# Kernel tuning notes

Measured on AMD Instinct MI355X. Metric: run time of the kernel, lower is better.

Reference implementation:

```python
import jax, jax.numpy as jnp
import numpy as np

B, S, A, E, H, V, P = 128, 256, 8, 300, 300, 50000, 3


def _gru(x, wih, whh, bih, bhh):
    """torch.nn.GRU (single layer, batch_first) with gate order r,z,n."""
    h0 = jnp.zeros((x.shape[0], whh.shape[1]), x.dtype)

    def step(h, xt):
        gi = xt @ wih.T + bih            # [B,3H]
        gh = h @ whh.T + bhh
        ir, iz, in_ = jnp.split(gi, 3, axis=-1)
        hr, hz, hn = jnp.split(gh, 3, axis=-1)
        r = jax.nn.sigmoid(ir + hr)
        z = jax.nn.sigmoid(iz + hz)
        n = jnp.tanh(in_ + r * hn)
        hnew = (1.0 - z) * n + z * h
        return hnew, hnew

    _, ys = jax.lax.scan(step, h0, jnp.swapaxes(x, 0, 1))  # scan over time
    return jnp.swapaxes(ys, 0, 1)                          # [B,S,H]


def setup_inputs() -> dict:
    key = jax.random.key(0)
    ks = jax.random.split(key, 16)
    rn = lambda k, shape, s=0.05: jax.random.normal(k, shape, jnp.float32) * s
    z = lambda *shape: jnp.zeros(shape, jnp.float32)
    return {
        "embed_table": rn(ks[0], (V, E), 1.0),
        "w1": rn(ks[1], (E, 3 * E)), "b1": z(E),
        "w2": rn(ks[2], (1, E)),
        "wm": rn(ks[3], (E, E)), "bm": z(E),
        "wd": rn(ks[4], (P, E)), "bd": z(P),
        "wih_l": rn(ks[5], (3 * H, E)), "whh_l": rn(ks[6], (3 * H, H)),
        "bih_l": z(3 * H), "bhh_l": z(3 * H),
        "wih_r": rn(ks[7], (3 * H, E)), "whh_r": rn(ks[8], (3 * H, H)),
        "bih_r": z(3 * H), "bhh_r": z(3 * H),
        "wml": rn(ks[9], (1, H)), "bml": z(1),
        "wmr": rn(ks[10], (1, H)), "bmr": z(1),
        # all token ids >= 1 so lengths are exactly the padded length (packing == identity)
        "text_raw_indices": jax.random.randint(ks[11], (B, S), 1, V),
        "aspect_indices": jax.random.randint(ks[12], (B, A), 1, V),
        "x_l": jax.random.randint(ks[13], (B, S), 1, V),
        "x_r": jax.random.randint(ks[14], (B, S), 1, V),
    }


def _forward(embed_table, w1, b1, w2, wm, bm, wd, bd,
             wih_l, whh_l, bih_l, bhh_l, wih_r, whh_r, bih_r, bhh_r,
             wml, bml, wmr, bmr, text, aspect, xl, xr):
    memory_len = jnp.sum(text != 0, -1)    # [B]
    aspect_len = jnp.sum(aspect != 0, -1)
    left_len = jnp.sum(xl != 0, -1)

    v_a = jnp.sum(embed_table[aspect], 1) / aspect_len[:, None].astype(jnp.float32)  # [B,E]
    memory = embed_table[text]             # [B,S,E]

    # ---- context attention (attention #1), fully vectorized ----
    ctx_l = _gru(embed_table[xl], wih_l, whh_l, bih_l, bhh_l)  # [B,S,H]
    ctx_r = _gru(embed_table[xr], wih_r, whh_r, bih_r, bhh_r)
    attn_l = jax.nn.sigmoid(jnp.einsum('bsh,h->bs', ctx_l, wml[0]) + bml[0]) + 0.5  # [B,S]
    attn_r = jax.nn.sigmoid(jnp.einsum('bsh,h->bs', ctx_r, wmr[0]) + bmr[0]) + 0.5

    idx = jnp.arange(S)[None, :]                      # [1,S]
    a_start = (left_len - aspect_len)[:, None]        # [B,1]
    a_end = left_len[:, None]
    # attn_r reversed over the first aspect_end positions: attn_rr[i,t] = attn_r[i, a_end-1-t]
    attn_rr = jnp.take_along_axis(attn_r, jnp.clip(a_end - 1 - idx, 0, S - 1), axis=1)
    # attn_l shifted by aspect_start: attn_ls[i,t] = attn_l[i, t - a_start]
    attn_ls = jnp.take_along_axis(attn_l, jnp.clip(idx - a_start, 0, S - 1), axis=1)
    w = jnp.where(idx < a_start, attn_rr,
                  jnp.where(idx < a_end, (attn_rr + attn_ls) * 0.5, attn_ls))
    w = jnp.where(idx < memory_len[:, None], w, 1.0)  # untouched past memory_len
    memory = memory * w[..., None]

    v_s = jnp.sum(memory, 1) / memory_len[:, None].astype(jnp.float32)  # [B,E]

    # ---- content attention (attention #2) ----
    feat = jnp.concatenate([memory,
                            jnp.broadcast_to(v_a[:, None, :], memory.shape),
                            jnp.broadcast_to(v_s[:, None, :], memory.shape)], -1)  # [B,S,3E]
    c = jnp.tanh(feat @ w1.T + b1) @ w2.T             # [B,S,1]
    alpha = jax.nn.softmax(c[..., 0], axis=1)         # [B,S]
    v_ts = jnp.einsum('bse,bs->be', memory, alpha)    # [B,E]

    v_ns = v_ts + v_s                                 # dropout is identity at eval
    v_ms = jnp.tanh(v_ns @ wm.T + bm)
    return jax.nn.softmax(v_ms @ wd.T + bd, axis=-1)  # [B,P]


def reference(embed_table, w1, b1, w2, wm, bm, wd, bd,
              wih_l, whh_l, bih_l, bhh_l, wih_r, whh_r, bih_r, bhh_r,
              wml, bml, wmr, bmr, text_raw_indices, aspect_indices, x_l, x_r):
    return _forward(embed_table, w1, b1, w2, wm, bm, wd, bd,
                    wih_l, whh_l, bih_l, bhh_l, wih_r, whh_r, bih_r, bhh_r,
                    wml, bml, wmr, bmr, text_raw_indices, aspect_indices, x_l, x_r)
```

## Files before the change

### kernel.cpp

```cpp
#include <hip/hip_runtime.h>
#include <hip/hip_bf16.h>
#include <math.h>

#define Bd 128
#define Sd 256
#define Ad 8
#define Ed 300
#define Hd 300
#define EP 320
#define Pd 3
#define UC 5
#define BG 8

typedef __attribute__((ext_vector_type(8))) short bfrag;
typedef __attribute__((ext_vector_type(4))) float f32x4;
typedef __attribute__((ext_vector_type(4))) int i32x4;

#define OFF_LENS   0u
#define OFF_FLAGS  4096u
#define OFF_VA     8192u
#define OFF_VS     172032u
#define OFF_U      335872u
#define OFF_ATTN   499712u
#define OFF_ALPHA  761856u
#define OFF_C      892928u
#define OFF_HF     1024000u
#define OFF_PART   1351680u
#define OFF_WF     11837440u
#define OFF_W1B    14295040u
#define OFF_XF     14499840u
#define OFF_MEMW   14499840u
#define WS_NEEDED  56442880u

__device__ __forceinline__ unsigned short f2bf(float f) {
    __hip_bfloat16 h = __float2bfloat16(f);
    return *reinterpret_cast<unsigned short*>(&h);
}
__device__ __forceinline__ float bf2f(unsigned short u) {
    __hip_bfloat16 h = *reinterpret_cast<__hip_bfloat16*>(&u);
    return __bfloat162float(h);
}
__device__ __forceinline__ float sigm(float x) {
    return __builtin_amdgcn_rcpf(1.f + __expf(-x));
}
__device__ __forceinline__ float fast_tanh(float x) {
    x = fminf(fmaxf(x, -15.f), 15.f);
    float e = __expf(2.f * x);
    return (e - 1.f) * __builtin_amdgcn_rcpf(e + 1.f);
}

__device__ __forceinline__ bfrag l2_load16b(const void* p) {
    bfrag v;
    asm volatile("global_load_dwordx4 %0, %1, off sc0"
                 : "=v"(v) : "v"(p) : "memory");
    return v;
}
__device__ __forceinline__ void l2_store16(void* p, i32x4 v) {
    asm volatile("global_store_dwordx4 %0, %1, off sc0"
                 :: "v"(p), "v"(v) : "memory");
}

__global__ void k_lengths(const int* __restrict__ text, const int* __restrict__ aspect,
                          const int* __restrict__ xl, int* __restrict__ lens) {
    int b = blockIdx.x;
    __shared__ int red[3];
    if (threadIdx.x < 3) red[threadIdx.x] = 0;
    __syncthreads();
    int t = threadIdx.x;
    if (t < Sd) {
        if (text[b*Sd + t] != 0) atomicAdd(&red[0], 1);
        if (xl[b*Sd + t]  != 0) atomicAdd(&red[2], 1);
    }
    if (t < Ad) { if (aspect[b*Ad + t] != 0) atomicAdd(&red[1], 1); }
    __syncthreads();
    if (t < 3) lens[b*4 + t] = red[t];
}

__global__ void k_va(const float* __restrict__ embed, const int* __restrict__ aspect,
                     const int* __restrict__ lens, float* __restrict__ va) {
    int b = blockIdx.x;
    __shared__ int aidx[Ad];
    if (threadIdx.x < Ad) aidx[threadIdx.x] = aspect[b*Ad + threadIdx.x];
    __syncthreads();
    float inv = 1.0f / (float)lens[b*4+1];
    for (int e = threadIdx.x; e < EP; e += blockDim.x) {
        float s = 0.f;
        if (e < Ed) {
            for (int a = 0; a < Ad; ++a) s += embed[(size_t)aidx[a]*Ed + e];
        }
        va[b*EP + e] = s * inv;
    }
}

__global__ void k_xf(const float* __restrict__ embed, const int* __restrict__ xl,
                     const int* __restrict__ xr, unsigned short* __restrict__ XF) {
    int side = blockIdx.x >> 8;
    int t = blockIdx.x & 255;
    const int* xs = side ? xr : xl;
    __shared__ int rows_s[Bd];
    if (threadIdx.x < Bd) rows_s[threadIdx.x] = xs[threadIdx.x*Sd + t];
    __syncthreads();
    unsigned short* dst = XF + ((size_t)(side*Sd + t))*40960;
    for (int v8 = threadIdx.x; v8 < 5120; v8 += 256) {
        int idx = v8 << 3;
        int bt = idx / 5120;
        int r1 = idx - bt*5120;
        int kt = r1 >> 9;
        int r2 = r1 & 511;
        int lane = r2 >> 3;
        int b = bt*16 + (lane & 15);
        int kk = kt*32 + (lane >> 4)*8;
        const float* src = embed + (size_t)rows_s[b]*Ed + kk;
        unsigned short tmp[8];
        if (kk + 8 <= Ed) {
            f32x4 f0 = *(const f32x4*)(src);
            f32x4 f1 = *(const f32x4*)(src + 4);
            #pragma unroll
            for (int j = 0; j < 4; ++j) { tmp[j] = f2bf(f0[j]); tmp[4+j] = f2bf(f1[j]); }
        } else {
            #pragma unroll
            for (int j = 0; j < 8; ++j)
                tmp[j] = (kk + j < Ed) ? f2bf(src[j]) : (unsigned short)0;
        }
        *(bfrag*)(dst + idx) = *(const bfrag*)tmp;
    }
}

__global__ void k_wfrag(const float* __restrict__ wih_l, const float* __restrict__ whh_l,
                        const float* __restrict__ wih_r, const float* __restrict__ whh_r,
                        unsigned short* __restrict__ WF) {
    int bid = blockIdx.x;
    int side = bid / 120;
    int r = bid - side*120;
    int mat = r / 60; r -= mat*60;
    int g = r / 20;
    int ut = r - g*20;
    const float* W = mat ? (side ? whh_r : whh_l) : (side ? wih_r : wih_l);
    unsigned short* dst = WF + (size_t)bid*5120;
    for (int v8 = threadIdx.x; v8 < 640; v8 += 256) {
        int idx = v8 << 3;
        int kt = idx >> 9;
        int r2 = idx & 511;
        int lane = r2 >> 3;
        int unit = ut*16 + (lane & 15);
        int kk = kt*32 + (lane >> 4)*8;
        unsigned short tmp[8];
        if (unit < Hd && kk + 8 <= Ed) {
            const float* src = W + (size_t)(g*Hd + unit)*Ed + kk;
            f32x4 f0 = *(const f32x4*)(src);
            f32x4 f1 = *(const f32x4*)(src + 4);
            #pragma unroll
            for (int j = 0; j < 4; ++j) { tmp[j] = f2bf(f0[j]); tmp[4+j] = f2bf(f1[j]); }
        } else {
            #pragma unroll
            for (int j = 0; j < 8; ++j) {
                float v = (unit < Hd && kk + j < Ed) ? W[(size_t)(g*Hd + unit)*Ed + kk + j] : 0.f;
                tmp[j] = f2bf(v);
            }
        }
        *(bfrag*)(dst + idx) = *(const bfrag*)tmp;
    }
}

__global__ void k_w1conv(const float* __restrict__ w1, unsigned short* __restrict__ w1b) {
    int idx = blockIdx.x*256 + threadIdx.x;
    if (idx >= EP*EP) return;
    int e = idx / EP, k = idx - e*EP;
    float v = (e < Ed && k < Ed) ? w1[(size_t)e*900 + k] : 0.f;
    w1b[idx] = f2bf(v);
}

__global__ __launch_bounds__(256, 1) void k_gru(
        const unsigned short* __restrict__ WF,
        const unsigned short* __restrict__ XF,
        const float* __restrict__ bih_l, const float* __restrict__ bhh_l,
        const float* __restrict__ bih_r, const float* __restrict__ bhh_r,
        const float* __restrict__ wml, const float* __restrict__ wmr,
        unsigned short* __restrict__ HF,
        float* __restrict__ part, int* __restrict__ flags) {
    int bg = blockIdx.x & 7;
    int r8 = blockIdx.x >> 3;
    int side = r8 & 1;
    int uc = r8 >> 1;
    int tid = threadIdx.x;
    int w = tid >> 6, lane = tid & 63, ul = lane & 15, lq = lane >> 4;
    int utg = uc*4 + w;
    int u = utg*16 + ul;

    const float* bih = side ? bih_r : bih_l;
    const float* bhh = side ? bhh_r : bhh_l;
    const float* wmv = side ? wmr : wml;

    float bR=0.f, bZ=0.f, bNI=0.f, bNH=0.f, wml_r=0.f;
    if (u < Hd) {
        bR = bih[u] + bhh[u];
        bZ = bih[Hd+u] + bhh[Hd+u];
        bNI = bih[2*Hd+u];
        bNH = bhh[2*Hd+u];
        wml_r = wmv[u];
    }

    bfrag wI[3][10], wH[3][10];
    #pragma unroll
    for (int g = 0; g < 3; ++g) {
        const unsigned short* pI = WF + ((size_t)((side*2+0)*3+g)*20 + utg)*5120 + lane*8;
        const unsigned short* pH = WF + ((size_t)((side*2+1)*3+g)*20 + utg)*5120 + lane*8;
        #pragma unroll
        for (int kt = 0; kt < 10; ++kt) {
            wI[g][kt] = *(const bfrag*)(pI + kt*512);
            wH[g][kt] = *(const bfrag*)(pH + kt*512);
        }
    }

    __shared__ __align__(16) unsigned short hn_s[1024];
    int* flgL2 = flags + (side*8 + bg)*16;
    int* flgIC = flags + 512 + (side*8 + bg)*16;
    unsigned short* hfb = HF + (size_t)((side*8 + bg)*2)*5120;
    const unsigned short* xbase = XF + ((size_t)side*Sd*8 + bg)*5120 + lane*8;

    bfrag xA[10], xB[10];
    #pragma unroll
    for (int kt = 0; kt < 10; ++kt)
        xA[kt] = *(const bfrag*)(xbase + 0 + kt*512);

    float hreg[4] = {0.f,0.f,0.f,0.f};
    const f32x4 zero4 = {0.f,0.f,0.f,0.f};

#define GRU_STEP(T, XIN, XOUT) do {                                            \
    f32x4 aR = zero4, aZ = zero4, aNI = zero4, aNH = zero4;                    \
    _Pragma("unroll")                                                          \
    for (int kt = 0; kt < 10; ++kt) {                                          \
        aR  = __builtin_amdgcn_mfma_f32_16x16x32_bf16(XIN[kt], wI[0][kt], aR, 0,0,0); \
        aZ  = __builtin_amdgcn_mfma_f32_16x16x32_bf16(XIN[kt], wI[1][kt], aZ, 0,0,0); \
        aNI = __builtin_amdgcn_mfma_f32_16x16x32_bf16(XIN[kt], wI[2][kt], aNI, 0,0,0); \
    }                                                                          \
    if ((T) > 0) {                                                             \
        if (w == 0) {                                                          \
            int iters = 0;                                                     \
            while (true) {                                                     \
                int v = (T);                                                   \
                if (lane < 2*UC)                                               \
                    v = __hip_atomic_fetch_add(flgL2 + lane, 0, __ATOMIC_RELAXED, __HIP_MEMORY_SCOPE_WORKGROUP); \
                if (__all(v >= (T))) break;                                    \
                if (((++iters) & 63) == 0) {                                   \
                    int vv = (T);                                              \
                    if (lane < 2*UC)                                           \
                        vv = __hip_atomic_load(flgIC + lane, __ATOMIC_RELAXED, __HIP_MEMORY_SCOPE_AGENT); \
                    if (__all(vv >= (T))) break;                               \
                }                                                              \
            }                                                                  \
        }                                                                      \
        __syncthreads();                                                       \
    }                                                                          \
    asm volatile("" ::: "memory");                                             \
    const unsigned short* hg = hfb + (size_t)((T) & 1)*5120 + lane*8;          \
    bfrag hf[10];                                                              \
    _Pragma("unroll")                                                          \
    for (int kt = 0; kt < 10; ++kt)                                            \
        hf[kt] = l2_load16b(hg + kt*512);                                      \
    asm volatile("s_waitcnt vmcnt(0)" ::: "memory");                           \
    __builtin_amdgcn_sched_barrier(0);                                         \
    _Pragma("unroll")                                                          \
    for (int kt = 0; kt < 10; ++kt) {                                          \
        aR  = __builtin_amdgcn_mfma_f32_16x16x32_bf16(hf[kt], wH[0][kt], aR, 0,0,0); \
        aZ  = __builtin_amdgcn_mfma_f32_16x16x32_bf16(hf[kt], wH[1][kt], aZ, 0,0,0); \
        aNH = __builtin_amdgcn_mfma_f32_16x16x32_bf16(hf[kt], wH[2][kt], aNH, 0,0,0); \
    }                                                                          \
    {                                                                          \
        int u_local = w*16 + ul;                                               \
        int kt_l = u_local >> 5, ko = u_local & 31;                            \
        _Pragma("unroll")                                                      \
        for (int i = 0; i < 4; ++i) {                                          \
            float rr = sigm(aR[i] + bR);                                       \
            float zz = sigm(aZ[i] + bZ);                                       \
            float nn = fast_tanh(aNI[i] + bNI + rr*(aNH[i] + bNH));            \
            float hv = (1.f - zz)*nn + zz*hreg[i];                             \
            hreg[i] = hv;                                                      \
            int rrow = lq*4 + i;                                               \
            hn_s[kt_l*512 + (rrow + ((ko>>3)<<4))*8 + (ko&7)] = f2bf(hv);      \
        }                                                                      \
    }                                                                          \
    __syncthreads();           \
    if (w < 2) {                                                               \
        unsigned short* hd = hfb + (size_t)(((T)+1) & 1)*5120 + uc*1024;       \
        l2_store16(hd + (size_t)tid*8, ((const i32x4*)hn_s)[tid]);             \
        asm volatile("s_waitcnt vmcnt(0)" ::: "memory");                       \
        if (lane == 0 && (T) < Sd-1) {                                         \
            __hip_atomic_fetch_add(flgL2 + uc*2 + w, 1, __ATOMIC_RELAXED, __HIP_MEMORY_SCOPE_WORKGROUP); \
            __hip_atomic_store(flgIC + uc*2 + w, (T)+1, __ATOMIC_RELAXED, __HIP_MEMORY_SCOPE_AGENT); \
        }                                                                      \
    }                                                                          \
    {                                                                          \
        int tn = ((T)+1 < Sd) ? (T)+1 : Sd-1;                                  \
        const unsigned short* xp = xbase + (size_t)tn*40960;                   \
        _Pragma("unroll")                                                      \
        for (int kt = 0; kt < 10; ++kt)                                        \
            XOUT[kt] = *(const bfrag*)(xp + kt*512);                           \
    }                                                                          \
    _Pragma("unroll")                                                          \
    for (int i = 0; i < 4; ++i) {                                              \
        float pv = hreg[i] * wml_r;                                            \
        pv += __shfl_xor(pv, 1, 64);                                           \
        pv += __shfl_xor(pv, 2, 64);                                           \
        pv += __shfl_xor(pv, 4, 64);                                           \
        pv += __shfl_xor(pv, 8, 64);                                           \
        if (ul == 0)                                                           \
            part[((size_t)((((side*8+bg)*UC + uc)*4 + w)*16) + lq*4 + i)*Sd + (T)] = pv; \
    }                                                                          \
} while (0)

    #pragma unroll 1
    for (int tt = 0; tt < Sd; tt += 2) {
        GRU_STEP(tt,   xA, xB);
        GRU_STEP(tt+1, xB, xA);
    }
#undef GRU_STEP
}

__global__ void k_attn(const float* __restrict__ part, const float* __restrict__ bml,
                       const float* __restrict__ bmr, float* __restrict__ attn) {
    int side = blockIdx.x >> 7;
    int b = blockIdx.x & 127;
    int bg = b >> 4, r = b & 15;
    int t = threadIdx.x;
    float s = 0.f;
    for (int c = 0; c < UC*4; ++c)
        s += part[((size_t)(((side*8+bg)*UC*4 + c)*16) + r)*Sd + t];
    float bias = side ? bmr[0] : bml[0];
    attn[(size_t)(side*Bd + b)*Sd + t] = sigm(s + bias) + 0.5f;
}

__global__ void k_wmem(const float* __restrict__ embed, const int* __restrict__ text,
                       const float* __restrict__ attn, const int* __restrict__ lens,
                       unsigned short* __restrict__ memw, float* __restrict__ vs) {
    int b = blockIdx.x;
    __shared__ float w_sh[Sd];
    __shared__ int text_s[Sd];
    int memlen = lens[b*4+0], asplen = lens[b*4+1], leftlen = lens[b*4+2];
    int a_start = leftlen - asplen, a_end = leftlen;
    const float* attl = attn + (size_t)b*Sd;
    const float* attr = attn + (size_t)(Bd + b)*Sd;
    if (threadIdx.x < Sd) {
        int i = threadIdx.x;
        int irr = a_end - 1 - i; irr = irr < 0 ? 0 : (irr > Sd-1 ? Sd-1 : irr);
        int ils = i - a_start;   ils = ils < 0 ? 0 : (ils > Sd-1 ? Sd-1 : ils);
        float arr_ = attr[irr], als = attl[ils];
        float w = (i < a_start) ? arr_ : ((i < a_end) ? 0.5f*(arr_+als) : als);
        if (i >= memlen) w = 1.0f;
        w_sh[i] = w;
        text_s[i] = text[b*Sd + i];
    }
    __syncthreads();
    int e = threadIdx.x;
    float acc = 0.f;
    float invm = 1.0f/(float)lens[b*4+0];
    for (int s = 0; s < Sd; ++s) {
        float v = (e < Ed) ? embed[(size_t)text_s[s]*Ed + e] : 0.f;
        float mw = v * w_sh[s];
        memw[((size_t)b*Sd + s)*EP + e] = f2bf(mw);
        acc += mw;
    }
    vs[b*EP + e] = acc * invm;
}

__global__ void k_u(const float* __restrict__ w1, const float* __restrict__ b1,
                    const float* __restrict__ va, const float* __restrict__ vs,
                    float* __restrict__ u) {
    int b = blockIdx.x;
    __shared__ float va_s[Ed], vs_s[Ed];
    for (int k = threadIdx.x; k < Ed; k += blockDim.x) {
        va_s[k] = va[b*EP+k];
        vs_s[k] = vs[b*EP+k];
    }
    __syncthreads();
    int e = threadIdx.x;
    if (e >= EP) return;
    float acc = 0.f;
    if (e < Ed) {
        acc = b1[e];
        const float* r = w1 + (size_t)e*900;
        for (int k = 0; k < Ed; ++k) acc += va_s[k]*r[300+k];
        for (int k = 0; k < Ed; ++k) acc += vs_s[k]*r[600+k];
    }
    u[b*EP + e] = acc;
}

__global__ __launch_bounds__(256) void k_c(const unsigned short* __restrict__ memw,
                   const unsigned short* __restrict__ w1b,
                   const float* __restrict__ u, const float* __restrict__ w2,
                   float* __restrict__ cout) {
    int b = blockIdx.x >> 2;
    int s0 = (blockIdx.x & 3) * 64;
    __shared__ __align__(16) unsigned short A_s[64*328];
    __shared__ __align__(16) unsigned short Bp_s[EP*32];
    __shared__ float u_s[EP], w2_s[EP];
    for (int i = threadIdx.x; i < EP; i += 256) {
        u_s[i] = u[b*EP + i];
        w2_s[i] = (i < Ed) ? w2[i] : 0.f;
    }
    const unsigned short* Ag = memw + ((size_t)b*Sd + s0)*EP;
    for (int c8 = threadIdx.x; c8 < 64*40; c8 += 256) {
        int r = c8 / 40, kk = (c8 - r*40)*8;
        *(bfrag*)(A_s + r*328 + kk) = *(const bfrag*)(Ag + (size_t)r*EP + kk);
    }

    int wave = threadIdx.x >> 6, lane = threadIdx.x & 63;
    int ul = lane & 15, lq = lane >> 4;
    const f32x4 zero4 = {0.f,0.f,0.f,0.f};
    f32x4 acc[20];
    #pragma unroll
    for (int n = 0; n < 20; ++n) acc[n] = zero4;

    for (int kp = 0; kp < 10; ++kp) {
        __syncthreads();
        for (int c8 = threadIdx.x; c8 < EP*4; c8 += 256) {
            int e = c8 >> 2, kk = (c8 & 3)*8;
            *(bfrag*)(Bp_s + e*32 + kk) = *(const bfrag*)(w1b + (size_t)e*EP + kp*32 + kk);
        }
        __syncthreads();
        bfrag a = *(const bfrag*)(A_s + (wave*16 + ul)*328 + kp*32 + lq*8);
        #pragma unroll
        for (int n = 0; n < 20; ++n) {
            bfrag bb = *(const bfrag*)(Bp_s + (n*16 + ul)*32 + lq*8);
            acc[n] = __builtin_amdgcn_mfma_f32_16x16x32_bf16(a, bb, acc[n], 0, 0, 0);
        }
    }
    float cs[4] = {0.f,0.f,0.f,0.f};
    #pragma unroll
    for (int n = 0; n < 20; ++n) {
        int e = n*16 + ul;
        #pragma unroll
        for (int i = 0; i < 4; ++i)
            cs[i] += w2_s[e] * fast_tanh(acc[n][i] + u_s[e]);
    }
    #pragma unroll
    for (int i = 0; i < 4; ++i) {
        float v = cs[i];
        v += __shfl_xor(v, 1, 64); v += __shfl_xor(v, 2, 64);
        v += __shfl_xor(v, 4, 64); v += __shfl_xor(v, 8, 64);
        if (ul == 0) cout[(size_t)b*Sd + s0 + wave*16 + lq*4 + i] = v;
    }
}

__global__ void k_alpha(const float* __restrict__ cin, float* __restrict__ alpha) {
    int b = blockIdx.x;
    int t = threadIdx.x;
    __shared__ float buf[Sd];
    float v = cin[(size_t)b*Sd + t];
    buf[t] = v; __syncthreads();
    for (int s2 = 128; s2 > 0; s2 >>= 1) {
        if (t < s2) buf[t] = fmaxf(buf[t], buf[t+s2]);
        __syncthreads();
    }
    float mx = buf[0];
    __syncthreads();
    float ex = __expf(v - mx);
    buf[t] = ex; __syncthreads();
    for (int s2 = 128; s2 > 0; s2 >>= 1) {
        if (t < s2) buf[t] += buf[t+s2];
        __syncthreads();
    }
    alpha[(size_t)b*Sd + t] = ex / buf[0];
}

__global__ void k_final(const unsigned short* __restrict__ memw, const float* __restrict__ alpha,
                        const float* __restrict__ vs, const float* __restrict__ wm,
                        const float* __restrict__ bm, const float* __restrict__ wd,
                        const float* __restrict__ bd, float* __restrict__ out) {
    int b = blockIdx.x;
    __shared__ float al_s[Sd];
    __shared__ float vns_s[Ed];
    __shared__ float vms_s[Ed];
    __shared__ float lg_s[Pd];
    if (threadIdx.x < Sd) al_s[threadIdx.x] = alpha[(size_t)b*Sd + threadIdx.x];
    __syncthreads();
    int e = threadIdx.x;
    if (e < Ed) {
        float acc = 0.f;
        const unsigned short* mp = memw + (size_t)b*Sd*EP + e;
        for (int s = 0; s < Sd; ++s) acc += bf2f(mp[(size_t)s*EP]) * al_s[s];
        vns_s[e] = acc + vs[b*EP + e];
    }
    __syncthreads();
    if (e < Ed) {
        float acc = bm[e];
        const float* r = wm + (size_t)e*Ed;
        for (int k = 0; k < Ed; ++k) acc += vns_s[k]*r[k];
        vms_s[e] = fast_tanh(acc);
    }
    __syncthreads();
    if (e < Pd) {
        float acc = bd[e];
        const float* r = wd + (size_t)e*Ed;
        for (int k = 0; k < Ed; ++k) acc += vms_s[k]*r[k];
        lg_s[e] = acc;
    }
    __syncthreads();
    if (e < Pd) {
        float m = fmaxf(lg_s[0], fmaxf(lg_s[1], lg_s[2]));
        float den = __expf(lg_s[0]-m)+__expf(lg_s[1]-m)+__expf(lg_s[2]-m);
        out[b*Pd + e] = __expf(lg_s[e]-m)/den;
    }
}

extern "C" void kernel_launch(void* const* d_in, const int* in_sizes, int n_in,
                              void* d_out, int out_size, void* d_ws, size_t ws_size,
                              hipStream_t stream) {
    const float* embed = (const float*)d_in[0];
    const float* w1    = (const float*)d_in[1];
    const float* b1    = (const float*)d_in[2];
    const float* w2    = (const float*)d_in[3];
    const float* wm    = (const float*)d_in[4];
    const float* bm    = (const float*)d_in[5];
    const float* wd    = (const float*)d_in[6];
    const float* bd    = (const float*)d_in[7];
    const float* wih_l = (const float*)d_in[8];
    const float* whh_l = (const float*)d_in[9];
    const float* bih_l = (const float*)d_in[10];
    const float* bhh_l = (const float*)d_in[11];
    const float* wih_r = (const float*)d_in[12];
    const float* whh_r = (const float*)d_in[13];
    const float* bih_r = (const float*)d_in[14];
    const float* bhh_r = (const float*)d_in[15];
    const float* wml   = (const float*)d_in[16];
    const float* bml   = (const float*)d_in[17];
    const float* wmr   = (const float*)d_in[18];
    const float* bmr   = (const float*)d_in[19];
    const int* text    = (const int*)d_in[20];
    const int* aspect  = (const int*)d_in[21];
    const int* xl      = (const int*)d_in[22];
    const int* xr      = (const int*)d_in[23];

    if (ws_size < (size_t)WS_NEEDED) return;
    char* ws = (char*)d_ws;
    int* lens            = (int*)(ws + OFF_LENS);
    int* flags           = (int*)(ws + OFF_FLAGS);
    float* va            = (float*)(ws + OFF_VA);
    float* vs            = (float*)(ws + OFF_VS);
    float* u             = (float*)(ws + OFF_U);
    float* attn          = (float*)(ws + OFF_ATTN);
    float* alpha         = (float*)(ws + OFF_ALPHA);
    float* c             = (float*)(ws + OFF_C);
    unsigned short* HF   = (unsigned short*)(ws + OFF_HF);
    float* part          = (float*)(ws + OFF_PART);
    unsigned short* WF   = (unsigned short*)(ws + OFF_WF);
    unsigned short* w1b  = (unsigned short*)(ws + OFF_W1B);
    unsigned short* XF   = (unsigned short*)(ws + OFF_XF);
    unsigned short* memw = (unsigned short*)(ws + OFF_MEMW);

    hipMemsetAsync(ws + OFF_FLAGS, 0, 4096, stream);
    hipMemsetAsync(ws + OFF_HF, 0, 327680, stream);

    k_lengths<<<128, 256, 0, stream>>>(text, aspect, xl, lens);
    k_va     <<<128, 320, 0, stream>>>(embed, aspect, lens, va);
    k_xf     <<<512, 256, 0, stream>>>(embed, xl, xr, XF);
    k_wfrag  <<<240, 256, 0, stream>>>(wih_l, whh_l, wih_r, whh_r, WF);
    k_w1conv <<<400, 256, 0, stream>>>(w1, w1b);
    k_gru    <<<80, 256, 0, stream>>>(WF, XF, bih_l, bhh_l, bih_r, bhh_r,
                                      wml, wmr, HF, part, flags);
    k_attn   <<<256, 256, 0, stream>>>(part, bml, bmr, attn);
    k_wmem   <<<128, 320, 0, stream>>>(embed, text, attn, lens, memw, vs);
    k_u      <<<128, 320, 0, stream>>>(w1, b1, va, vs, u);
    k_c      <<<512, 256, 0, stream>>>(memw, w1b, u, w2, c);
    k_alpha  <<<128, 256, 0, stream>>>(c, alpha);
    k_final  <<<128, 320, 0, stream>>>(memw, alpha, vs, wm, bm, wd, bd, (float*)d_out);
}
```

Measured before the change: 821.1 us.

## Use single step counter, double-buffered LDS for own hidden slice, direct B loads in k_c

Result: slower. 898.6 us (+9.4%).

```diff
diff --git a/kernel.cpp b/kernel.cpp
--- a/kernel.cpp
+++ b/kernel.cpp
@@ -212,8 +212,12 @@
         }
     }
 
-    __shared__ __align__(16) unsigned short hn_s[1024];
-    int* flgL2 = flags + (side*8 + bg)*16;
+    __shared__ __align__(16) unsigned short hn_s[2][1024];
+    for (int i = tid; i < 512; i += 256)
+        ((unsigned long long*)hn_s)[i] = 0ull;
+    __syncthreads();
+
+    int* ctrL2 = flags + (side*8 + bg)*16 + 10;
     int* flgIC = flags + 512 + (side*8 + bg)*16;
     unsigned short* hfb = HF + (size_t)((side*8 + bg)*2)*5120;
     const unsigned short* xbase = XF + ((size_t)side*Sd*8 + bg)*5120 + lane*8;
@@ -226,7 +230,7 @@
     float hreg[4] = {0.f,0.f,0.f,0.f};
     const f32x4 zero4 = {0.f,0.f,0.f,0.f};
 
-#define GRU_STEP(T, XIN, XOUT) do {                                            \
+#define GRU_STEP(T, PAR, XIN, XOUT) do {                                       \
     f32x4 aR = zero4, aZ = zero4, aNI = zero4, aNH = zero4;                    \
     _Pragma("unroll")                                                          \
     for (int kt = 0; kt < 10; ++kt) {                                          \
@@ -236,15 +240,16 @@
     }                                                                          \
     if ((T) > 0) {                                                             \
         if (w == 0) {                                                          \
+            int target = 10*(T);                                               \
             int iters = 0;                                                     \
             while (true) {                                                     \
-                int v = (T);                                                   \
-                if (lane < 2*UC)                                               \
-                    v = __hip_atomic_fetch_add(flgL2 + lane, 0, __ATOMIC_RELAXED, __HIP_MEMORY_SCOPE_WORKGROUP); \
-                if (__all(v >= (T))) break;                                    \
+                int v = target;                                                \
+                if (lane == 0)                                                 \
+                    v = __hip_atomic_fetch_add(ctrL2, 0, __ATOMIC_RELAXED, __HIP_MEMORY_SCOPE_WORKGROUP); \
+                if (__all(v >= target)) break;                                 \
                 if (((++iters) & 63) == 0) {                                   \
                     int vv = (T);                                              \
-                    if (lane < 2*UC)                                           \
+                    if (lane < 10)                                             \
                         vv = __hip_atomic_load(flgIC + lane, __ATOMIC_RELAXED, __HIP_MEMORY_SCOPE_AGENT); \
                     if (__all(vv >= (T))) break;                               \
                 }                                                              \
@@ -253,11 +258,16 @@
         __syncthreads();                                                       \
     }                                                                          \
     asm volatile("" ::: "memory");                                             \
-    const unsigned short* hg = hfb + (size_t)((T) & 1)*5120 + lane*8;          \
+    const unsigned short* hg = hfb + (size_t)(PAR)*5120 + lane*8;              \
     bfrag hf[10];                                                              \
     _Pragma("unroll")                                                          \
     for (int kt = 0; kt < 10; ++kt)                                            \
-        hf[kt] = l2_load16b(hg + kt*512);                                      \
+        if ((kt >> 1) != uc)                                                   \
+            hf[kt] = l2_load16b(hg + kt*512);                                  \
+    _Pragma("unroll")                                                          \
+    for (int kt = 0; kt < 10; ++kt)                                            \
+        if ((kt >> 1) == uc)                                                   \
+            hf[kt] = *(const bfrag*)(&hn_s[(PAR)^1][(kt & 1)*512 + lane*8]);   \
     asm volatile("s_waitcnt vmcnt(0)" ::: "memory");                           \
     __builtin_amdgcn_sched_barrier(0);                                         \
     _Pragma("unroll")                                                          \
@@ -277,16 +287,16 @@
             float hv = (1.f - zz)*nn + zz*hreg[i];                             \
             hreg[i] = hv;                                                      \
             int rrow = lq*4 + i;                                               \
-            hn_s[kt_l*512 + (rrow + ((ko>>3)<<4))*8 + (ko&7)] = f2bf(hv);      \
+            hn_s[PAR][kt_l*512 + (rrow + ((ko>>3)<<4))*8 + (ko&7)] = f2bf(hv); \
         }                                                                      \
     }                                                                          \
-    __syncthreads();           \
+    __syncthreads();      \
     if (w < 2) {                                                               \
-        unsigned short* hd = hfb + (size_t)(((T)+1) & 1)*5120 + uc*1024;       \
-        l2_store16(hd + (size_t)tid*8, ((const i32x4*)hn_s)[tid]);             \
+        unsigned short* hd = hfb + (size_t)((PAR)^1)*5120 + uc*1024;           \
+        l2_store16(hd + (size_t)tid*8, ((const i32x4*)hn_s[PAR])[tid]);        \
         asm volatile("s_waitcnt vmcnt(0)" ::: "memory");                       \
         if (lane == 0 && (T) < Sd-1) {                                         \
-            __hip_atomic_fetch_add(flgL2 + uc*2 + w, 1, __ATOMIC_RELAXED, __HIP_MEMORY_SCOPE_WORKGROUP); \
+            __hip_atomic_fetch_add(ctrL2, 1, __ATOMIC_RELAXED, __HIP_MEMORY_SCOPE_WORKGROUP); \
             __hip_atomic_store(flgIC + uc*2 + w, (T)+1, __ATOMIC_RELAXED, __HIP_MEMORY_SCOPE_AGENT); \
         }                                                                      \
     }                                                                          \
@@ -311,8 +321,8 @@
 
     #pragma unroll 1
     for (int tt = 0; tt < Sd; tt += 2) {
-        GRU_STEP(tt,   xA, xB);
-        GRU_STEP(tt+1, xB, xA);
+        GRU_STEP(tt,   0, xA, xB);
+        GRU_STEP(tt+1, 1, xB, xA);
     }
 #undef GRU_STEP
 }
@@ -392,7 +402,6 @@
     int b = blockIdx.x >> 2;
     int s0 = (blockIdx.x & 3) * 64;
     __shared__ __align__(16) unsigned short A_s[64*328];
-    __shared__ __align__(16) unsigned short Bp_s[EP*32];
     __shared__ float u_s[EP], w2_s[EP];
     for (int i = threadIdx.x; i < EP; i += 256) {
         u_s[i] = u[b*EP + i];
@@ -403,6 +412,7 @@
         int r = c8 / 40, kk = (c8 - r*40)*8;
         *(bfrag*)(A_s + r*328 + kk) = *(const bfrag*)(Ag + (size_t)r*EP + kk);
     }
+    __syncthreads();
 
     int wave = threadIdx.x >> 6, lane = threadIdx.x & 63;
     int ul = lane & 15, lq = lane >> 4;
@@ -412,18 +422,14 @@
     for (int n = 0; n < 20; ++n) acc[n] = zero4;
 
     for (int kp = 0; kp < 10; ++kp) {
-        __syncthreads();
-        for (int c8 = threadIdx.x; c8 < EP*4; c8 += 256) {
-            int e = c8 >> 2, kk = (c8 & 3)*8;
-            *(bfrag*)(Bp_s + e*32 + kk) = *(const bfrag*)(w1b + (size_t)e*EP + kp*32 + kk);
-        }
-        __syncthreads();
         bfrag a = *(const bfrag*)(A_s + (wave*16 + ul)*328 + kp*32 + lq*8);
+        bfrag bb[20];
         #pragma unroll
-        for (int n = 0; n < 20; ++n) {
-            bfrag bb = *(const bfrag*)(Bp_s + (n*16 + ul)*32 + lq*8);
-            acc[n] = __builtin_amdgcn_mfma_f32_16x16x32_bf16(a, bb, acc[n], 0, 0, 0);
-        }
+        for (int n = 0; n < 20; ++n)
+            bb[n] = *(const bfrag*)(w1b + (size_t)(n*16 + ul)*EP + kp*32 + lq*8);
+        #pragma unroll
+        for (int n = 0; n < 20; ++n)
+            acc[n] = __builtin_amdgcn_mfma_f32_16x16x32_bf16(a, bb[n], acc[n], 0, 0, 0);
     }
     float cs[4] = {0.f,0.f,0.f,0.f};
     #pragma unroll
```

## Fuse small pre/post GRU kernels to cut launches and intermediate buffers

Applied to the files above, without the earlier changes.

Measured after the change: 808.9 us. No clear change (-1.5%).

```diff
diff --git a/kernel.cpp b/kernel.cpp
--- a/kernel.cpp
+++ b/kernel.cpp
@@ -21,8 +21,6 @@
 #define OFF_VA     8192u
 #define OFF_VS     172032u
 #define OFF_U      335872u
-#define OFF_ATTN   499712u
-#define OFF_ALPHA  761856u
 #define OFF_C      892928u
 #define OFF_HF     1024000u
 #define OFF_PART   1351680u
@@ -60,10 +58,12 @@
                  :: "v"(p), "v"(v) : "memory");
 }
 
-__global__ void k_lengths(const int* __restrict__ text, const int* __restrict__ aspect,
-                          const int* __restrict__ xl, int* __restrict__ lens) {
+__global__ void k_lenva(const float* __restrict__ embed, const int* __restrict__ text,
+                        const int* __restrict__ aspect, const int* __restrict__ xl,
+                        int* __restrict__ lens, float* __restrict__ va) {
     int b = blockIdx.x;
     __shared__ int red[3];
+    __shared__ int aidx[Ad];
     if (threadIdx.x < 3) red[threadIdx.x] = 0;
     __syncthreads();
     int t = threadIdx.x;
@@ -71,25 +71,19 @@
         if (text[b*Sd + t] != 0) atomicAdd(&red[0], 1);
         if (xl[b*Sd + t]  != 0) atomicAdd(&red[2], 1);
     }
-    if (t < Ad) { if (aspect[b*Ad + t] != 0) atomicAdd(&red[1], 1); }
+    if (t < Ad) {
+        aidx[t] = aspect[b*Ad + t];
+        if (aidx[t] != 0) atomicAdd(&red[1], 1);
+    }
     __syncthreads();
     if (t < 3) lens[b*4 + t] = red[t];
-}
-
-__global__ void k_va(const float* __restrict__ embed, const int* __restrict__ aspect,
-                     const int* __restrict__ lens, float* __restrict__ va) {
-    int b = blockIdx.x;
-    __shared__ int aidx[Ad];
-    if (threadIdx.x < Ad) aidx[threadIdx.x] = aspect[b*Ad + threadIdx.x];
-    __syncthreads();
-    float inv = 1.0f / (float)lens[b*4+1];
-    for (int e = threadIdx.x; e < EP; e += blockDim.x) {
-        float s = 0.f;
-        if (e < Ed) {
-            for (int a = 0; a < Ad; ++a) s += embed[(size_t)aidx[a]*Ed + e];
-        }
-        va[b*EP + e] = s * inv;
-    }
+    float inv = 1.0f / (float)red[1];
+    int e = t;
+    float s = 0.f;
+    if (e < Ed) {
+        for (int a = 0; a < Ad; ++a) s += embed[(size_t)aidx[a]*Ed + e];
+    }
+    va[b*EP + e] = s * inv;
 }
 
 __global__ void k_xf(const float* __restrict__ embed, const int* __restrict__ xl,
@@ -317,72 +311,69 @@
 #undef GRU_STEP
 }
 
-__global__ void k_attn(const float* __restrict__ part, const float* __restrict__ bml,
-                       const float* __restrict__ bmr, float* __restrict__ attn) {
-    int side = blockIdx.x >> 7;
-    int b = blockIdx.x & 127;
+__global__ void k_awu(const float* __restrict__ part, const float* __restrict__ bml,
+                      const float* __restrict__ bmr, const float* __restrict__ embed,
+                      const int* __restrict__ text, const int* __restrict__ lens,
+                      const float* __restrict__ w1, const float* __restrict__ b1,
+                      const float* __restrict__ va,
+                      unsigned short* __restrict__ memw, float* __restrict__ vs,
+                      float* __restrict__ u) {
+    int b = blockIdx.x;
     int bg = b >> 4, r = b & 15;
-    int t = threadIdx.x;
-    float s = 0.f;
-    for (int c = 0; c < UC*4; ++c)
-        s += part[((size_t)(((side*8+bg)*UC*4 + c)*16) + r)*Sd + t];
-    float bias = side ? bmr[0] : bml[0];
-    attn[(size_t)(side*Bd + b)*Sd + t] = sigm(s + bias) + 0.5f;
-}
-
-__global__ void k_wmem(const float* __restrict__ embed, const int* __restrict__ text,
-                       const float* __restrict__ attn, const int* __restrict__ lens,
-                       unsigned short* __restrict__ memw, float* __restrict__ vs) {
-    int b = blockIdx.x;
+    __shared__ float attl_s[Sd], attr_s[Sd];
     __shared__ float w_sh[Sd];
     __shared__ int text_s[Sd];
+    __shared__ float va_s[EP], vs_s[EP];
+    int t = threadIdx.x;
+
+    if (t < Sd) {
+        float sl = 0.f, sr = 0.f;
+        for (int c = 0; c < UC*4; ++c) {
+            sl += part[((size_t)(((0*8+bg)*UC*4 + c)*16) + r)*Sd + t];
+            sr += part[((size_t)(((1*8+bg)*UC*4 + c)*16) + r)*Sd + t];
+        }
+        attl_s[t] = sigm(sl + bml[0]) + 0.5f;
+        attr_s[t] = sigm(sr + bmr[0]) + 0.5f;
+        text_s[t] = text[b*Sd + t];
+    }
+    va_s[t] = va[b*EP + t];
+    __syncthreads();
+
     int memlen = lens[b*4+0], asplen = lens[b*4+1], leftlen = lens[b*4+2];
     int a_start = leftlen - asplen, a_end = leftlen;
-    const float* attl = attn + (size_t)b*Sd;
-    const float* attr = attn + (size_t)(Bd + b)*Sd;
-    if (threadIdx.x < Sd) {
-        int i = threadIdx.x;
+    if (t < Sd) {
+        int i = t;
         int irr = a_end - 1 - i; irr = irr < 0 ? 0 : (irr > Sd-1 ? Sd-1 : irr);
         int ils = i - a_start;   ils = ils < 0 ? 0 : (ils > Sd-1 ? Sd-1 : ils);
-        float arr_ = attr[irr], als = attl[ils];
+        float arr_ = attr_s[irr], als = attl_s[ils];
         float w = (i < a_start) ? arr_ : ((i < a_end) ? 0.5f*(arr_+als) : als);
         if (i >= memlen) w = 1.0f;
         w_sh[i] = w;
-        text_s[i] = text[b*Sd + i];
-    }
-    __syncthreads();
-    int e = threadIdx.x;
+    }
+    __syncthreads();
+
+    int e = t;
     float acc = 0.f;
-    float invm = 1.0f/(float)lens[b*4+0];
+    float invm = 1.0f/(float)memlen;
     for (int s = 0; s < Sd; ++s) {
         float v = (e < Ed) ? embed[(size_t)text_s[s]*Ed + e] : 0.f;
         float mw = v * w_sh[s];
         memw[((size_t)b*Sd + s)*EP + e] = f2bf(mw);
         acc += mw;
     }
-    vs[b*EP + e] = acc * invm;
-}
-
-__global__ void k_u(const float* __restrict__ w1, const float* __restrict__ b1,
-                    const float* __restrict__ va, const float* __restrict__ vs,
-                    float* __restrict__ u) {
-    int b = blockIdx.x;
-    __shared__ float va_s[Ed], vs_s[Ed];
-    for (int k = threadIdx.x; k < Ed; k += blockDim.x) {
-        va_s[k] = va[b*EP+k];
-        vs_s[k] = vs[b*EP+k];
-    }
-    __syncthreads();
-    int e = threadIdx.x;
-    if (e >= EP) return;
-    float acc = 0.f;
+    float vsv = acc * invm;
+    vs[b*EP + e] = vsv;
+    vs_s[e] = vsv;
+    __syncthreads();
+
+    float accu = 0.f;
     if (e < Ed) {
-        acc = b1[e];
-        const float* r = w1 + (size_t)e*900;
-        for (int k = 0; k < Ed; ++k) acc += va_s[k]*r[300+k];
-        for (int k = 0; k < Ed; ++k) acc += vs_s[k]*r[600+k];
-    }
-    u[b*EP + e] = acc;
+        accu = b1[e];
+        const float* rw = w1 + (size_t)e*900;
+        for (int k = 0; k < Ed; ++k) accu += va_s[k]*rw[300+k];
+        for (int k = 0; k < Ed; ++k) accu += vs_s[k]*rw[600+k];
+    }
+    u[b*EP + e] = accu;
 }
 
 __global__ __launch_bounds__(256) void k_c(const unsigned short* __restrict__ memw,
@@ -442,39 +433,38 @@
     }
 }
 
-__global__ void k_alpha(const float* __restrict__ cin, float* __restrict__ alpha) {
+__global__ void k_af(const float* __restrict__ cin, const unsigned short* __restrict__ memw,
+                     const float* __restrict__ vs, const float* __restrict__ wm,
+                     const float* __restrict__ bm, const float* __restrict__ wd,
+                     const float* __restrict__ bd, float* __restrict__ out) {
     int b = blockIdx.x;
     int t = threadIdx.x;
     __shared__ float buf[Sd];
-    float v = cin[(size_t)b*Sd + t];
-    buf[t] = v; __syncthreads();
-    for (int s2 = 128; s2 > 0; s2 >>= 1) {
-        if (t < s2) buf[t] = fmaxf(buf[t], buf[t+s2]);
-        __syncthreads();
-    }
-    float mx = buf[0];
-    __syncthreads();
-    float ex = __expf(v - mx);
-    buf[t] = ex; __syncthreads();
-    for (int s2 = 128; s2 > 0; s2 >>= 1) {
-        if (t < s2) buf[t] += buf[t+s2];
-        __syncthreads();
-    }
-    alpha[(size_t)b*Sd + t] = ex / buf[0];
-}
-
-__global__ void k_final(const unsigned short* __restrict__ memw, const float* __restrict__ alpha,
-                        const float* __restrict__ vs, const float* __restrict__ wm,
-                        const float* __restrict__ bm, const float* __restrict__ wd,
-                        const float* __restrict__ bd, float* __restrict__ out) {
-    int b = blockIdx.x;
     __shared__ float al_s[Sd];
     __shared__ float vns_s[Ed];
     __shared__ float vms_s[Ed];
     __shared__ float lg_s[Pd];
-    if (threadIdx.x < Sd) al_s[threadIdx.x] = alpha[(size_t)b*Sd + threadIdx.x];
-    __syncthreads();
-    int e = threadIdx.x;
+
+    float v = 0.f;
+    if (t < Sd) { v = cin[(size_t)b*Sd + t]; buf[t] = v; }
+    __syncthreads();
+    for (int s2 = 128; s2 > 0; s2 >>= 1) {
+        if (t < s2) buf[t] = fmaxf(buf[t], buf[t+s2]);
+        __syncthreads();
+    }
+    float mx = buf[0];
+    __syncthreads();
+    float ex = 0.f;
+    if (t < Sd) { ex = __expf(v - mx); buf[t] = ex; }
+    __syncthreads();
+    for (int s2 = 128; s2 > 0; s2 >>= 1) {
+        if (t < s2) buf[t] += buf[t+s2];
+        __syncthreads();
+    }
+    if (t < Sd) al_s[t] = ex / buf[0];
+    __syncthreads();
+
+    int e = t;
     if (e < Ed) {
         float acc = 0.f;
         const unsigned short* mp = memw + (size_t)b*Sd*EP + e;
@@ -538,8 +528,6 @@
     float* va            = (float*)(ws + OFF_VA);
     float* vs            = (float*)(ws + OFF_VS);
     float* u             = (float*)(ws + OFF_U);
-    float* attn          = (float*)(ws + OFF_ATTN);
-    float* alpha         = (float*)(ws + OFF_ALPHA);
     float* c             = (float*)(ws + OFF_C);
     unsigned short* HF   = (unsigned short*)(ws + OFF_HF);
     float* part          = (float*)(ws + OFF_PART);
@@ -551,17 +539,14 @@
     hipMemsetAsync(ws + OFF_FLAGS, 0, 4096, stream);
     hipMemsetAsync(ws + OFF_HF, 0, 327680, stream);
 
-    k_lengths<<<128, 256, 0, stream>>>(text, aspect, xl, lens);
-    k_va     <<<128, 320, 0, stream>>>(embed, aspect, lens, va);
+    k_lenva  <<<128, 320, 0, stream>>>(embed, text, aspect, xl, lens, va);
     k_xf     <<<512, 256, 0, stream>>>(embed, xl, xr, XF);
     k_wfrag  <<<240, 256, 0, stream>>>(wih_l, whh_l, wih_r, whh_r, WF);
     k_w1conv <<<400, 256, 0, stream>>>(w1, w1b);
     k_gru    <<<80, 256, 0, stream>>>(WF, XF, bih_l, bhh_l, bih_r, bhh_r,
                                       wml, wmr, HF, part, flags);
-    k_attn   <<<256, 256, 0, stream>>>(part, bml, bmr, attn);
-    k_wmem   <<<128, 320, 0, stream>>>(embed, text, attn, lens, memw, vs);
-    k_u      <<<128, 320, 0, stream>>>(w1, b1, va, vs, u);
+    k_awu    <<<128, 320, 0, stream>>>(part, bml, bmr, embed, text, lens,
+                                       w1, b1, va, memw, vs, u);
     k_c      <<<512, 256, 0, stream>>>(memw, w1b, u, w2, c);
-    k_alpha  <<<128, 256, 0, stream>>>(c, alpha);
-    k_final  <<<128, 320, 0, stream>>>(memw, alpha, vs, wm, bm, wd, bd, (float*)d_out);
-}
+    k_af     <<<128, 320, 0, stream>>>(c, memw, vs, wm, bm, wd, bd, (float*)d_out);
+}
```
